# Kernel optimization log

Measured on AMD Instinct MI355X. Metric: run time of the kernel, lower is better.

Reference implementation:

```python
import jax, jax.numpy as jnp
import numpy as np
from jax import lax

HALF = 0.5    # box bound |w_i| <= 0.5 (hardcoded in the torch module)
CAP = 0.1     # |sum(w)| <= 0.1
BISECT_ITERS = 60


def _project(mu):
    """Exact solution of: min ||w-mu||^2 s.t. |sum w|<=CAP, -HALF<=w<=HALF.
    This is what the CvxpyLayer (ADMM/SCS) solves; we use the KKT closed form:
    w = clip(mu - lam, -HALF, HALF) with scalar lam per row chosen so that
    sum(w) = clip(sum(clip(mu)), -CAP, CAP). lam found by bisection (non-diff),
    then recomputed in closed form over the active set for exact implicit grads.
    mu: [B, N] -> w: [B, N]
    """
    w0 = jnp.clip(mu, -HALF, HALF)
    s0 = jnp.sum(w0, axis=-1, keepdims=True)          # [B,1]
    t = jnp.clip(s0, -CAP, CAP)                       # target row sum

    # --- bisection for lam* (gradients stopped; g(lam) is decreasing) ---
    mu_sg = lax.stop_gradient(mu)
    t_sg = lax.stop_gradient(t)
    lo = jnp.min(mu_sg, axis=-1, keepdims=True) - (HALF + CAP)
    hi = jnp.max(mu_sg, axis=-1, keepdims=True) + (HALF + CAP)

    def body(i, lh):
        lo, hi = lh
        mid = 0.5 * (lo + hi)
        g = jnp.sum(jnp.clip(mu_sg - mid, -HALF, HALF), axis=-1, keepdims=True)
        too_big = g > t_sg            # sum too large -> need larger lam
        return jnp.where(too_big, mid, lo), jnp.where(too_big, hi, mid)

    lo, hi = lax.fori_loop(0, BISECT_ITERS, body, (lo, hi))
    lam_star = 0.5 * (lo + hi)                        # [B,1], no grads

    # --- closed-form lam over the active set (exact implicit gradient) ---
    z = mu_sg - lam_star
    active = (z > -HALF) & (z < HALF)
    n_act = jnp.sum(active, axis=-1, keepdims=True).astype(mu.dtype)
    n_hi = jnp.sum(z >= HALF, axis=-1, keepdims=True).astype(mu.dtype)
    n_lo = jnp.sum(z <= -HALF, axis=-1, keepdims=True).astype(mu.dtype)
    sum_act = jnp.sum(jnp.where(active, mu, jnp.zeros_like(mu)), axis=-1, keepdims=True)
    lam = (sum_act + HALF * (n_hi - n_lo) - t) / jnp.maximum(n_act, 1.0)
    lam = jnp.where(n_act > 0, lam, lam_star)
    return jnp.clip(mu - lam, -HALF, HALF)


def setup_inputs() -> dict:
    key = jax.random.key(0)
    x = jax.random.normal(key, (262144, 128), dtype=jnp.float32)
    return {"x": x}


def reference(x):
    return _project(x)
```

## Files before the change

kernel.cpp:

```cpp
#include <hip/hip_runtime.h>

#define HALFB 0.5f
#define CAPB  0.1f

__device__ __forceinline__ float clip05(float z) {
    return fminf(fmaxf(z, -HALFB), HALFB);
}

template <int CTRL>
__device__ __forceinline__ float dppf(float v) {
    return __int_as_float(__builtin_amdgcn_update_dpp(
        __float_as_int(v), __float_as_int(v), CTRL, 0xF, 0xF, false));
}
__device__ __forceinline__ float red8f(float v) {
    v += dppf<0xB1>(v); v += dppf<0x4E>(v); v += dppf<0x141>(v); return v;
}
__device__ __forceinline__ float min8f(float v) {
    v = fminf(v, dppf<0xB1>(v)); v = fminf(v, dppf<0x4E>(v));
    v = fminf(v, dppf<0x141>(v)); return v;
}
__device__ __forceinline__ float max8f(float v) {
    v = fmaxf(v, dppf<0xB1>(v)); v = fmaxf(v, dppf<0x4E>(v));
    v = fmaxf(v, dppf<0x141>(v)); return v;
}

__global__ __launch_bounds__(256, 4) void proj_kernel(
    const float* __restrict__ x, float* __restrict__ out, int nrows)
{
    const int lane = threadIdx.x & 63;
    const int wid  = (blockIdx.x << 2) | (threadIdx.x >> 6);
    const int q    = lane & 7;
    int row = (wid << 3) | (lane >> 3);
    if (row >= nrows) row = nrows - 1;

    const float4* __restrict__ px = (const float4*)x  + ((size_t)row << 5) + q;
    float4*       __restrict__ po = (float4*)out      + ((size_t)row << 5) + q;

    float4 v[4];
    #pragma unroll
    for (int j = 0; j < 4; ++j) v[j] = px[j << 3];

    float s0a = 0.f, s0b = 0.f, s0c = 0.f, s0d = 0.f;
    float naa = 0.f, nab = 0.f, nac = 0.f, nad = 0.f;
    float mna = 3.0e38f, mnb = 3.0e38f, mxa = -3.0e38f, mxb = -3.0e38f;
    #pragma unroll
    for (int j = 0; j < 4; ++j) {
        s0a += clip05(v[j].x); s0b += clip05(v[j].y);
        s0c += clip05(v[j].z); s0d += clip05(v[j].w);
        naa += (fabsf(v[j].x) < HALFB) ? 1.f : 0.f;
        nab += (fabsf(v[j].y) < HALFB) ? 1.f : 0.f;
        nac += (fabsf(v[j].z) < HALFB) ? 1.f : 0.f;
        nad += (fabsf(v[j].w) < HALFB) ? 1.f : 0.f;
        mna = fminf(mna, fminf(v[j].x, v[j].y));
        mnb = fminf(mnb, fminf(v[j].z, v[j].w));
        mxa = fmaxf(mxa, fmaxf(v[j].x, v[j].y));
        mxb = fmaxf(mxb, fmaxf(v[j].z, v[j].w));
    }
    float g  = red8f((s0a + s0b) + (s0c + s0d));
    float na = red8f((naa + nab) + (nac + nad));
    const float vmn = min8f(fminf(mna, mnb));
    const float vmx = max8f(fmaxf(mxa, mxb));

    const float t = fminf(fmaxf(g, -CAPB), CAPB);
    float lo  = vmn - (HALFB + CAPB);
    float hi  = vmx + (HALFB + CAPB);
    float lam = 0.f;

    for (int it = 0; it < 20; ++it) {
        if (fabsf(g - t) <= 1e-4f) break;
        if (g > t) lo = lam; else hi = lam;
        float ln;
        if (na > 0.f) {
            ln = lam + (g - t) * __builtin_amdgcn_rcpf(na);
            if (!(ln > lo && ln < hi)) ln = 0.5f * (lo + hi);
        } else {
            ln = 0.5f * (lo + hi);
        }
        if (ln == lam) break;
        lam = ln;

        float ga = 0.f, gb = 0.f, gc = 0.f, gd = 0.f;
        float pa = 0.f, pb = 0.f, pc = 0.f, pd = 0.f;
        #pragma unroll
        for (int j = 0; j < 4; ++j) {
            const float z0 = v[j].x - lam, z1 = v[j].y - lam;
            const float z2 = v[j].z - lam, z3 = v[j].w - lam;
            ga += clip05(z0); gb += clip05(z1);
            gc += clip05(z2); gd += clip05(z3);
            pa += (fabsf(z0) < HALFB) ? 1.f : 0.f;
            pb += (fabsf(z1) < HALFB) ? 1.f : 0.f;
            pc += (fabsf(z2) < HALFB) ? 1.f : 0.f;
            pd += (fabsf(z3) < HALFB) ? 1.f : 0.f;
        }
        g  = red8f((ga + gb) + (gc + gd));
        na = red8f((pa + pb) + (pc + pd));
    }

    const float lam_f = (na > 0.f) ? lam + (g - t) / na : lam;

    #pragma unroll
    for (int j = 0; j < 4; ++j) {
        po[j << 3] = make_float4(clip05(v[j].x - lam_f), clip05(v[j].y - lam_f),
                                 clip05(v[j].z - lam_f), clip05(v[j].w - lam_f));
    }
}

extern "C" void kernel_launch(void* const* d_in, const int* in_sizes, int n_in,
                              void* d_out, int out_size, void* d_ws, size_t ws_size,
                              hipStream_t stream) {
    const float* x = (const float*)d_in[0];
    float* out     = (float*)d_out;
    const int nrows = out_size / 128;
    const int grid  = (nrows + 31) / 32;
    hipLaunchKernelGGL(proj_kernel, dim3(grid), dim3(256), 0, stream, x, out, nrows);
}
```

Before: 45.40 us.

## Add warp-specialized producer waves staging input rows through double-buffered LDS

The kernel splits each block into two producer waves that load global rows into a double-buffered shared-memory tile and four consumer waves that run the projection on rows read from LDS. Each block now handles 256 rows over 8 stages, with barriers between stages. The aim is to overlap global loads with the iterative solve and keep more bytes in flight. In exchange it adds an LDS round trip and per-stage barriers, and it drops the tail guard: the grid is nrows/256, so leftover rows are skipped when nrows is not a multiple of 256.

```diff
diff --git a/kernel.cpp b/kernel.cpp
--- a/kernel.cpp
+++ b/kernel.cpp
@@ -2,6 +2,7 @@
 
 #define HALFB 0.5f
 #define CAPB  0.1f
+#define NSTAGE 8
 
 __device__ __forceinline__ float clip05(float z) {
     return fminf(fmaxf(z, -HALFB), HALFB);
@@ -24,84 +25,127 @@
     v = fmaxf(v, dppf<0x141>(v)); return v;
 }
 
-__global__ __launch_bounds__(256, 4) void proj_kernel(
+__global__ __launch_bounds__(384, 6) void proj_kernel(
     const float* __restrict__ x, float* __restrict__ out, int nrows)
 {
-    const int lane = threadIdx.x & 63;
-    const int wid  = (blockIdx.x << 2) | (threadIdx.x >> 6);
-    const int q    = lane & 7;
-    int row = (wid << 3) | (lane >> 3);
-    if (row >= nrows) row = nrows - 1;
+    __shared__ float4 tile[2][1024];
 
-    const float4* __restrict__ px = (const float4*)x  + ((size_t)row << 5) + q;
-    float4*       __restrict__ po = (float4*)out      + ((size_t)row << 5) + q;
+    const int tid  = threadIdx.x;
+    const int lane = tid & 63;
+    const int w    = tid >> 6;
+    const size_t brow = (size_t)blockIdx.x * (32 * NSTAGE);
 
-    float4 v[4];
-    #pragma unroll
-    for (int j = 0; j < 4; ++j) v[j] = px[j << 3];
+    if (w >= 4) {
+        const int m = w - 4;
+        const float4* __restrict__ gsrc = (const float4*)x + (brow << 5);
+        const int lofs = (m << 9) + lane;
 
-    float s0a = 0.f, s0b = 0.f, s0c = 0.f, s0d = 0.f;
-    float naa = 0.f, nab = 0.f, nac = 0.f, nad = 0.f;
-    float mna = 3.0e38f, mnb = 3.0e38f, mxa = -3.0e38f, mxb = -3.0e38f;
-    #pragma unroll
-    for (int j = 0; j < 4; ++j) {
-        s0a += clip05(v[j].x); s0b += clip05(v[j].y);
-        s0c += clip05(v[j].z); s0d += clip05(v[j].w);
-        naa += (fabsf(v[j].x) < HALFB) ? 1.f : 0.f;
-        nab += (fabsf(v[j].y) < HALFB) ? 1.f : 0.f;
-        nac += (fabsf(v[j].z) < HALFB) ? 1.f : 0.f;
-        nad += (fabsf(v[j].w) < HALFB) ? 1.f : 0.f;
-        mna = fminf(mna, fminf(v[j].x, v[j].y));
-        mnb = fminf(mnb, fminf(v[j].z, v[j].w));
-        mxa = fmaxf(mxa, fmaxf(v[j].x, v[j].y));
-        mxb = fmaxf(mxb, fmaxf(v[j].z, v[j].w));
-    }
-    float g  = red8f((s0a + s0b) + (s0c + s0d));
-    float na = red8f((naa + nab) + (nac + nad));
-    const float vmn = min8f(fminf(mna, mnb));
-    const float vmx = max8f(fmaxf(mxa, mxb));
+        float4 buf[8];
+        #pragma unroll
+        for (int i = 0; i < 8; ++i)
+            buf[i] = gsrc[lofs + (i << 6)];
 
-    const float t = fminf(fmaxf(g, -CAPB), CAPB);
-    float lo  = vmn - (HALFB + CAPB);
-    float hi  = vmx + (HALFB + CAPB);
-    float lam = 0.f;
+        for (int s = 0; s < NSTAGE; ++s) {
+            float4* __restrict__ dst = &tile[s & 1][0];
+            #pragma unroll
+            for (int i = 0; i < 8; ++i)
+                dst[lofs + (i << 6)] = buf[i];
+            asm volatile("s_waitcnt lgkmcnt(0)" ::: "memory");
+            if (s + 1 < NSTAGE) {
+                const float4* __restrict__ gn = gsrc + ((size_t)(s + 1) << 10);
+                #pragma unroll
+                for (int i = 0; i < 8; ++i)
+                    buf[i] = gn[lofs + (i << 6)];
+            }
+            __builtin_amdgcn_s_barrier();
+            asm volatile("" ::: "memory");
+            __builtin_amdgcn_s_barrier();
+            asm volatile("" ::: "memory");
+        }
+    } else {
+        const int q    = lane & 7;
+        const int rloc = lane >> 3;
+        const int srow = (w << 3) + rloc;
 
-    for (int it = 0; it < 20; ++it) {
-        if (fabsf(g - t) <= 1e-4f) break;
-        if (g > t) lo = lam; else hi = lam;
-        float ln;
-        if (na > 0.f) {
-            ln = lam + (g - t) * __builtin_amdgcn_rcpf(na);
-            if (!(ln > lo && ln < hi)) ln = 0.5f * (lo + hi);
-        } else {
-            ln = 0.5f * (lo + hi);
+        for (int s = 0; s < NSTAGE; ++s) {
+            __builtin_amdgcn_s_barrier();
+            asm volatile("" ::: "memory");
+
+            const float4* __restrict__ src = &tile[s & 1][0];
+            float4 v[4];
+            #pragma unroll
+            for (int j = 0; j < 4; ++j)
+                v[j] = src[(srow << 5) + (j << 3) + q];
+
+            float s0a = 0.f, s0b = 0.f, s0c = 0.f, s0d = 0.f;
+            float naa = 0.f, nab = 0.f, nac = 0.f, nad = 0.f;
+            float mna = 3.0e38f, mnb = 3.0e38f, mxa = -3.0e38f, mxb = -3.0e38f;
+            #pragma unroll
+            for (int j = 0; j < 4; ++j) {
+                s0a += clip05(v[j].x); s0b += clip05(v[j].y);
+                s0c += clip05(v[j].z); s0d += clip05(v[j].w);
+                naa += (fabsf(v[j].x) < HALFB) ? 1.f : 0.f;
+                nab += (fabsf(v[j].y) < HALFB) ? 1.f : 0.f;
+                nac += (fabsf(v[j].z) < HALFB) ? 1.f : 0.f;
+                nad += (fabsf(v[j].w) < HALFB) ? 1.f : 0.f;
+                mna = fminf(mna, fminf(v[j].x, v[j].y));
+                mnb = fminf(mnb, fminf(v[j].z, v[j].w));
+                mxa = fmaxf(mxa, fmaxf(v[j].x, v[j].y));
+                mxb = fmaxf(mxb, fmaxf(v[j].z, v[j].w));
+            }
+            float g  = red8f((s0a + s0b) + (s0c + s0d));
+            float na = red8f((naa + nab) + (nac + nad));
+            const float vmn = min8f(fminf(mna, mnb));
+            const float vmx = max8f(fmaxf(mxa, mxb));
+
+            const float t = fminf(fmaxf(g, -CAPB), CAPB);
+            float lo  = vmn - (HALFB + CAPB);
+            float hi  = vmx + (HALFB + CAPB);
+            float lam = 0.f;
+
+            for (int it = 0; it < 20; ++it) {
+                if (fabsf(g - t) <= 1e-4f) break;
+                if (g > t) lo = lam; else hi = lam;
+                float ln;
+                if (na > 0.f) {
+                    ln = lam + (g - t) * __builtin_amdgcn_rcpf(na);
+                    if (!(ln > lo && ln < hi)) ln = 0.5f * (lo + hi);
+                } else {
+                    ln = 0.5f * (lo + hi);
+                }
+                if (ln == lam) break;
+                lam = ln;
+
+                float ga = 0.f, gb = 0.f, gc = 0.f, gd = 0.f;
+                float pa = 0.f, pb = 0.f, pc = 0.f, pd = 0.f;
+                #pragma unroll
+                for (int j = 0; j < 4; ++j) {
+                    const float z0 = v[j].x - lam, z1 = v[j].y - lam;
+                    const float z2 = v[j].z - lam, z3 = v[j].w - lam;
+                    ga += clip05(z0); gb += clip05(z1);
+                    gc += clip05(z2); gd += clip05(z3);
+                    pa += (fabsf(z0) < HALFB) ? 1.f : 0.f;
+                    pb += (fabsf(z1) < HALFB) ? 1.f : 0.f;
+                    pc += (fabsf(z2) < HALFB) ? 1.f : 0.f;
+                    pd += (fabsf(z3) < HALFB) ? 1.f : 0.f;
+                }
+                g  = red8f((ga + gb) + (gc + gd));
+                na = red8f((pa + pb) + (pc + pd));
+            }
+
+            const float lam_f = (na > 0.f) ? lam + (g - t) / na : lam;
+
+            const size_t grow = brow + (size_t)(s << 5) + srow;
+            float4* __restrict__ po = (float4*)out + (grow << 5) + q;
+            #pragma unroll
+            for (int j = 0; j < 4; ++j)
+                po[j << 3] = make_float4(
+                    clip05(v[j].x - lam_f), clip05(v[j].y - lam_f),
+                    clip05(v[j].z - lam_f), clip05(v[j].w - lam_f));
+
+            __builtin_amdgcn_s_barrier();
+            asm volatile("" ::: "memory");
         }
-        if (ln == lam) break;
-        lam = ln;
-
-        float ga = 0.f, gb = 0.f, gc = 0.f, gd = 0.f;
-        float pa = 0.f, pb = 0.f, pc = 0.f, pd = 0.f;
-        #pragma unroll
-        for (int j = 0; j < 4; ++j) {
-            const float z0 = v[j].x - lam, z1 = v[j].y - lam;
-            const float z2 = v[j].z - lam, z3 = v[j].w - lam;
-            ga += clip05(z0); gb += clip05(z1);
-            gc += clip05(z2); gd += clip05(z3);
-            pa += (fabsf(z0) < HALFB) ? 1.f : 0.f;
-            pb += (fabsf(z1) < HALFB) ? 1.f : 0.f;
-            pc += (fabsf(z2) < HALFB) ? 1.f : 0.f;
-            pd += (fabsf(z3) < HALFB) ? 1.f : 0.f;
-        }
-        g  = red8f((ga + gb) + (gc + gd));
-        na = red8f((pa + pb) + (pc + pd));
-    }
-
-    const float lam_f = (na > 0.f) ? lam + (g - t) / na : lam;
-
-    #pragma unroll
-    for (int j = 0; j < 4; ++j) {
-        po[j << 3] = make_float4(clip05(v[j].x - lam_f), clip05(v[j].y - lam_f),
-                                 clip05(v[j].z - lam_f), clip05(v[j].w - lam_f));
     }
 }
 
@@ -111,6 +155,6 @@
     const float* x = (const float*)d_in[0];
     float* out     = (float*)d_out;
     const int nrows = out_size / 128;
-    const int grid  = (nrows + 31) / 32;
-    hipLaunchKernelGGL(proj_kernel, dim3(grid), dim3(256), 0, stream, x, out, nrows);
+    const int grid  = nrows / (32 * NSTAGE);
+    hipLaunchKernelGGL(proj_kernel, dim3(grid), dim3(384), 0, stream, x, out, nrows);
 }
```

Result: slower. 88.93 us (+95.9%).

## Make waves persistent over 8 row batches with double-buffered global-to-LDS loads

Applied to the files above, without the earlier changes.

Each wave now handles 8 consecutive batches of 8 rows. The next batch is prefetched straight into LDS through global_load_lds while the current batch is solved, and vmcnt waits order the buffers. The aim is to hide global load latency behind the iterative Newton/bisection solve and to cut launch and tail overhead by using 8x fewer blocks. The cost is 32KB of LDS per block, which may limit occupancy, plus an extra LDS read per element. The grid now assumes nrows is divisible by 256 and no longer clamps out-of-range rows.

```diff
diff --git a/kernel.cpp b/kernel.cpp
--- a/kernel.cpp
+++ b/kernel.cpp
@@ -2,6 +2,7 @@
 
 #define HALFB 0.5f
 #define CAPB  0.1f
+#define NB 8
 
 __device__ __forceinline__ float clip05(float z) {
     return fminf(fmaxf(z, -HALFB), HALFB);
@@ -27,81 +28,114 @@
 __global__ __launch_bounds__(256, 4) void proj_kernel(
     const float* __restrict__ x, float* __restrict__ out, int nrows)
 {
-    const int lane = threadIdx.x & 63;
-    const int wid  = (blockIdx.x << 2) | (threadIdx.x >> 6);
+    __shared__ float4 tile[2048];
+
+    const int tid  = threadIdx.x;
+    const int lane = tid & 63;
+    const int w    = tid >> 6;
     const int q    = lane & 7;
-    int row = (wid << 3) | (lane >> 3);
-    if (row >= nrows) row = nrows - 1;
+    const int rloc = lane >> 3;
 
-    const float4* __restrict__ px = (const float4*)x  + ((size_t)row << 5) + q;
-    float4*       __restrict__ po = (float4*)out      + ((size_t)row << 5) + q;
+    const size_t wrow0 = ((size_t)(blockIdx.x * 4 + w)) * (8 * NB);
+    const float4* __restrict__ gsrc = (const float4*)x + (wrow0 << 5);
+    float4*       __restrict__ gdst = (float4*)out     + (wrow0 << 5);
+    const int wbase = w << 9;
 
-    float4 v[4];
     #pragma unroll
-    for (int j = 0; j < 4; ++j) v[j] = px[j << 3];
+    for (int i = 0; i < 4; ++i)
+        __builtin_amdgcn_global_load_lds(
+            (const __attribute__((address_space(1))) void*)(gsrc + (i << 6) + lane),
+            (__attribute__((address_space(3))) void*)(&tile[wbase + (i << 6)]),
+            16, 0, 0);
 
-    float s0a = 0.f, s0b = 0.f, s0c = 0.f, s0d = 0.f;
-    float naa = 0.f, nab = 0.f, nac = 0.f, nad = 0.f;
-    float mna = 3.0e38f, mnb = 3.0e38f, mxa = -3.0e38f, mxb = -3.0e38f;
-    #pragma unroll
-    for (int j = 0; j < 4; ++j) {
-        s0a += clip05(v[j].x); s0b += clip05(v[j].y);
-        s0c += clip05(v[j].z); s0d += clip05(v[j].w);
-        naa += (fabsf(v[j].x) < HALFB) ? 1.f : 0.f;
-        nab += (fabsf(v[j].y) < HALFB) ? 1.f : 0.f;
-        nac += (fabsf(v[j].z) < HALFB) ? 1.f : 0.f;
-        nad += (fabsf(v[j].w) < HALFB) ? 1.f : 0.f;
-        mna = fminf(mna, fminf(v[j].x, v[j].y));
-        mnb = fminf(mnb, fminf(v[j].z, v[j].w));
-        mxa = fmaxf(mxa, fmaxf(v[j].x, v[j].y));
-        mxb = fmaxf(mxb, fmaxf(v[j].z, v[j].w));
-    }
-    float g  = red8f((s0a + s0b) + (s0c + s0d));
-    float na = red8f((naa + nab) + (nac + nad));
-    const float vmn = min8f(fminf(mna, mnb));
-    const float vmx = max8f(fmaxf(mxa, mxb));
+    for (int s = 0; s < NB; ++s) {
+        const int slot = s & 1;
 
-    const float t = fminf(fmaxf(g, -CAPB), CAPB);
-    float lo  = vmn - (HALFB + CAPB);
-    float hi  = vmx + (HALFB + CAPB);
-    float lam = 0.f;
+        if (s + 1 < NB) {
+            const float4* g = gsrc + ((size_t)(s + 1) << 8);
+            float4* l = &tile[wbase + ((slot ^ 1) << 8)];
+            #pragma unroll
+            for (int i = 0; i < 4; ++i)
+                __builtin_amdgcn_global_load_lds(
+                    (const __attribute__((address_space(1))) void*)(g + (i << 6) + lane),
+                    (__attribute__((address_space(3))) void*)(l + (i << 6)),
+                    16, 0, 0);
+            asm volatile("s_waitcnt vmcnt(4)" ::: "memory");
+        } else {
+            asm volatile("s_waitcnt vmcnt(0)" ::: "memory");
+        }
+        __builtin_amdgcn_sched_barrier(0);
 
-    for (int it = 0; it < 20; ++it) {
-        if (fabsf(g - t) <= 1e-4f) break;
-        if (g > t) lo = lam; else hi = lam;
-        float ln;
-        if (na > 0.f) {
-            ln = lam + (g - t) * __builtin_amdgcn_rcpf(na);
-            if (!(ln > lo && ln < hi)) ln = 0.5f * (lo + hi);
-        } else {
-            ln = 0.5f * (lo + hi);
-        }
-        if (ln == lam) break;
-        lam = ln;
+        const float4* src = &tile[wbase + (slot << 8)];
+        float4 v[4];
+        #pragma unroll
+        for (int j = 0; j < 4; ++j)
+            v[j] = src[(rloc << 5) + (j << 3) + q];
 
-        float ga = 0.f, gb = 0.f, gc = 0.f, gd = 0.f;
-        float pa = 0.f, pb = 0.f, pc = 0.f, pd = 0.f;
+        float s0a = 0.f, s0b = 0.f, s0c = 0.f, s0d = 0.f;
+        float naa = 0.f, nab = 0.f, nac = 0.f, nad = 0.f;
+        float mna = 3.0e38f, mnb = 3.0e38f, mxa = -3.0e38f, mxb = -3.0e38f;
         #pragma unroll
         for (int j = 0; j < 4; ++j) {
-            const float z0 = v[j].x - lam, z1 = v[j].y - lam;
-            const float z2 = v[j].z - lam, z3 = v[j].w - lam;
-            ga += clip05(z0); gb += clip05(z1);
-            gc += clip05(z2); gd += clip05(z3);
-            pa += (fabsf(z0) < HALFB) ? 1.f : 0.f;
-            pb += (fabsf(z1) < HALFB) ? 1.f : 0.f;
-            pc += (fabsf(z2) < HALFB) ? 1.f : 0.f;
-            pd += (fabsf(z3) < HALFB) ? 1.f : 0.f;
+            s0a += clip05(v[j].x); s0b += clip05(v[j].y);
+            s0c += clip05(v[j].z); s0d += clip05(v[j].w);
+            naa += (fabsf(v[j].x) < HALFB) ? 1.f : 0.f;
+            nab += (fabsf(v[j].y) < HALFB) ? 1.f : 0.f;
+            nac += (fabsf(v[j].z) < HALFB) ? 1.f : 0.f;
+            nad += (fabsf(v[j].w) < HALFB) ? 1.f : 0.f;
+            mna = fminf(mna, fminf(v[j].x, v[j].y));
+            mnb = fminf(mnb, fminf(v[j].z, v[j].w));
+            mxa = fmaxf(mxa, fmaxf(v[j].x, v[j].y));
+            mxb = fmaxf(mxb, fmaxf(v[j].z, v[j].w));
         }
-        g  = red8f((ga + gb) + (gc + gd));
-        na = red8f((pa + pb) + (pc + pd));
-    }
+        float g  = red8f((s0a + s0b) + (s0c + s0d));
+        float na = red8f((naa + nab) + (nac + nad));
+        const float vmn = min8f(fminf(mna, mnb));
+        const float vmx = max8f(fmaxf(mxa, mxb));
 
-    const float lam_f = (na > 0.f) ? lam + (g - t) / na : lam;
+        const float t = fminf(fmaxf(g, -CAPB), CAPB);
+        float lo  = vmn - (HALFB + CAPB);
+        float hi  = vmx + (HALFB + CAPB);
+        float lam = 0.f;
 
-    #pragma unroll
-    for (int j = 0; j < 4; ++j) {
-        po[j << 3] = make_float4(clip05(v[j].x - lam_f), clip05(v[j].y - lam_f),
-                                 clip05(v[j].z - lam_f), clip05(v[j].w - lam_f));
+        for (int it = 0; it < 20; ++it) {
+            if (fabsf(g - t) <= 1e-4f) break;
+            if (g > t) lo = lam; else hi = lam;
+            float ln;
+            if (na > 0.f) {
+                ln = lam + (g - t) * __builtin_amdgcn_rcpf(na);
+                if (!(ln > lo && ln < hi)) ln = 0.5f * (lo + hi);
+            } else {
+                ln = 0.5f * (lo + hi);
+            }
+            if (ln == lam) break;
+            lam = ln;
+
+            float ga = 0.f, gb = 0.f, gc = 0.f, gd = 0.f;
+            float pa = 0.f, pb = 0.f, pc = 0.f, pd = 0.f;
+            #pragma unroll
+            for (int j = 0; j < 4; ++j) {
+                const float z0 = v[j].x - lam, z1 = v[j].y - lam;
+                const float z2 = v[j].z - lam, z3 = v[j].w - lam;
+                ga += clip05(z0); gb += clip05(z1);
+                gc += clip05(z2); gd += clip05(z3);
+                pa += (fabsf(z0) < HALFB) ? 1.f : 0.f;
+                pb += (fabsf(z1) < HALFB) ? 1.f : 0.f;
+                pc += (fabsf(z2) < HALFB) ? 1.f : 0.f;
+                pd += (fabsf(z3) < HALFB) ? 1.f : 0.f;
+            }
+            g  = red8f((ga + gb) + (gc + gd));
+            na = red8f((pa + pb) + (pc + pd));
+        }
+
+        const float lam_f = (na > 0.f) ? lam + (g - t) / na : lam;
+
+        float4* po = gdst + ((size_t)s << 8);
+        #pragma unroll
+        for (int j = 0; j < 4; ++j)
+            po[(rloc << 5) + (j << 3) + q] = make_float4(
+                clip05(v[j].x - lam_f), clip05(v[j].y - lam_f),
+                clip05(v[j].z - lam_f), clip05(v[j].w - lam_f));
     }
 }
 
@@ -111,6 +145,6 @@
     const float* x = (const float*)d_in[0];
     float* out     = (float*)d_out;
     const int nrows = out_size / 128;
-    const int grid  = (nrows + 31) / 32;
+    const int grid  = nrows / (4 * 8 * NB);
     hipLaunchKernelGGL(proj_kernel, dim3(grid), dim3(256), 0, stream, x, out, nrows);
 }
```

After: 50.28 us. +10.8%, slower.
